# Performance work log

Hardware: AMD Instinct MI355X
Metric: run time of the kernel (lower is better)

Reference implementation:

```python
import jax, jax.numpy as jnp
import numpy as np
from jax import lax


def setup_inputs() -> dict:
    key = jax.random.key(0)
    kx, kw = jax.random.split(key)
    x = jax.random.normal(kx, (32, 3, 8192), dtype=jnp.float32)
    weight = jax.random.normal(kw, (128, 3, 64), dtype=jnp.float32)
    return {"x": x, "weight": weight}


def reference(x, weight):
    # x: [B, C, L], weight: [O, C, K]
    K = weight.shape[2]
    # Cross-correlation (conv1d, no bias, valid padding): [B, O, L-K+1]
    conv_out = lax.conv_general_dilated(
        x, weight, window_strides=(1,), padding='VALID',
        dimension_numbers=('NCH', 'OIH', 'NCH'))
    # Half squared norm of each shapelet: [O]
    w_norm = jnp.sum(weight ** 2, axis=(1, 2)) / 2
    # Half squared norm of each length-K window, via cumulative sums
    # (avoids materializing the [B, C, W, K] unfold tensor)
    sq = jnp.sum(x ** 2, axis=1)               # [B, L]
    c = jnp.pad(jnp.cumsum(sq, axis=1), ((0, 0), (1, 0)))  # [B, L+1]
    win_norm = (c[:, K:] - c[:, :-K]) / 2      # [B, L-K+1]
    # features = conv_out - (||w||^2/2 + ||window||^2/2)
    features = conv_out - w_norm[None, :, None] - win_norm[:, None, :]
    # global max-pool over time, then *(-2) -> min squared distance
    return -2.0 * jnp.max(features, axis=-1)   # [B, O]
```

## Files before the change

### kernel.cpp

```cpp
#include <hip/hip_runtime.h>
#include <hip/hip_bf16.h>
#include <float.h>

#define BB 32
#define LL 8192
#define OO 128
#define KK 64
#define WW (LL - KK + 1)
#define TCX 16

typedef __attribute__((ext_vector_type(8))) short short8;
typedef __attribute__((ext_vector_type(4))) float f32x4;

union AB { int4 i4; int i[4]; short8 v; };

static __device__ __forceinline__ unsigned int pkbf(float a, float b) {
    union { __hip_bfloat162 h; unsigned int u; } cv;
    cv.h = __float22bfloat162_rn(make_float2(a, b));
    return cv.u;
}

__global__ __launch_bounds__(256) void prep_kernel(const float* __restrict__ w,
                                                   unsigned short* __restrict__ wswz,
                                                   float* __restrict__ wn,
                                                   float* __restrict__ out) {
    int g = blockIdx.x * 256 + threadIdx.x;
    if (g < 3072) {
        int ob = g / 768;
        int rem = g - ob * 768;
        int rr = rem >> 5, o2 = rem & 31;
        int ks = rr >> 2, qp = rr & 3;
        int c = ks >> 1, h = ks & 1;
        const float* p = w + (size_t)(ob * 32 + o2) * 192 + c * 64 + h * 32 + qp * 8;
        float4 v0 = *(const float4*)p, v1 = *(const float4*)(p + 4);
        int4 pk;
        pk.x = (int)pkbf(v0.x, v0.y);
        pk.y = (int)pkbf(v0.z, v0.w);
        pk.z = (int)pkbf(v1.x, v1.y);
        pk.w = (int)pkbf(v1.z, v1.w);
        ((int4*)wswz)[g] = pk;
    }
    int oo = g - 3072;
    if (oo >= 0 && oo < OO) {
        const float* p = w + oo * 192;
        float s = 0.f;
        for (int i = 0; i < 192; ++i) { float v = p[i]; s = fmaf(v, v, s); }
        wn[oo] = 0.5f * s;
    }
    int oi = g - 3200;
    if (oi >= 0 && oi < BB * OO) out[oi] = 3.389e38f;
}

__global__ __launch_bounds__(256, 4) void shapeconv_main(const float* __restrict__ x,
                                                         const unsigned short* __restrict__ wswz,
                                                         const float* __restrict__ wn,
                                                         float* __restrict__ out) {
    __shared__ __align__(16) unsigned short w_lds[6144];
    __shared__ __align__(16) unsigned short xw_lds[4][576];
    __shared__ __align__(16) float sq_lds[4][192];
    __shared__ __align__(16) float P_lds[4][24];

    const int tcx = blockIdx.x;
    const int ob = blockIdx.y;
    const int b  = blockIdx.z;
    const int tid = threadIdx.x;
    const int wv = tid >> 6;
    const int lane = tid & 63;
    const int n  = lane & 15;
    const int qp = lane >> 4;
    const int T0w = (tcx * 4 + wv) * 128;

    float2 va[3], vb[3];
    const float* xb = x + (size_t)b * 3 * LL;
    {
        int e0 = T0w + 2 * lane;
        #pragma unroll
        for (int c = 0; c < 3; ++c) va[c] = *(const float2*)(xb + c * LL + e0);
        #pragma unroll
        for (int c = 0; c < 3; ++c) vb[c] = make_float2(0.f, 0.f);
        int e1 = T0w + 128 + 2 * lane;
        if (lane < 32 && e1 < LL) {
            #pragma unroll
            for (int c = 0; c < 3; ++c) vb[c] = *(const float2*)(xb + c * LL + e1);
        }
    }

    {
        const char* src = (const char*)wswz + (size_t)ob * 12288 + tid * 16;
        #pragma unroll
        for (int i = 0; i < 3; ++i) {
            __builtin_amdgcn_global_load_lds(
                (const __attribute__((address_space(1))) unsigned int*)(src + i * 4096),
                (__attribute__((address_space(3))) unsigned int*)((char*)w_lds + tid * 16 + i * 4096),
                16, 0, 0);
        }
    }

    float nw[2][4];
    #pragma unroll
    for (int ot = 0; ot < 2; ++ot)
        #pragma unroll
        for (int rg = 0; rg < 4; ++rg)
            nw[ot][rg] = wn[ob * 32 + 16 * ot + 4 * qp + rg];

    unsigned short* xw = xw_lds[wv];
    float* sqw = sq_lds[wv];
    float* Pw  = P_lds[wv];
    {
        float sx = 0.f, sy = 0.f;
        #pragma unroll
        for (int c = 0; c < 3; ++c) {
            *(unsigned int*)(xw + c * 192 + 2 * lane) = pkbf(va[c].x, va[c].y);
            sx = fmaf(va[c].x, va[c].x, sx);
            sy = fmaf(va[c].y, va[c].y, sy);
        }
        *(float2*)(sqw + 2 * lane) = make_float2(sx, sy);
        float p2 = sx + sy;
        p2 += __shfl_xor(p2, 1, 64);
        p2 += __shfl_xor(p2, 2, 64);
        if ((lane & 3) == 0) Pw[lane >> 2] = p2;
        float tx = 0.f, ty = 0.f;
        unsigned int pk[3];
        #pragma unroll
        for (int c = 0; c < 3; ++c) {
            tx = fmaf(vb[c].x, vb[c].x, tx);
            ty = fmaf(vb[c].y, vb[c].y, ty);
            pk[c] = pkbf(vb[c].x, vb[c].y);
        }
        if (lane < 32) {
            #pragma unroll
            for (int c = 0; c < 3; ++c) *(unsigned int*)(xw + c * 192 + 128 + 2 * lane) = pk[c];
            *(float2*)(sqw + 128 + 2 * lane) = make_float2(tx, ty);
        }
        float q2 = tx + ty;
        q2 += __shfl_xor(q2, 1, 64);
        q2 += __shfl_xor(q2, 2, 64);
        if (lane < 32 && (lane & 3) == 0) Pw[16 + (lane >> 2)] = q2;
    }

    __syncthreads();

    float wl[8];
    {
        float S = 0.f;
        #pragma unroll
        for (int i = 0; i < 8; ++i) S += Pw[n + i];
        #pragma unroll
        for (int r = 0; r < 8; ++r) {
            wl[r] = (T0w + 8 * n + r < WW) ? 0.5f * S : 1e30f;
            if (r < 7) S += sqw[8 * n + 64 + r] - sqw[8 * n + r];
        }
    }

    f32x4 acc[2][8];
    #pragma unroll
    for (int ot = 0; ot < 2; ++ot)
        #pragma unroll
        for (int rg = 0; rg < 4; ++rg)
            #pragma unroll
            for (int r = 0; r < 8; ++r)
                acc[ot][r][rg] = -nw[ot][rg] - wl[r];

    __builtin_amdgcn_s_setprio(1);
    #pragma unroll
    for (int ks = 0; ks < 6; ++ks) {
        int c = ks >> 1, h = ks & 1;
        int e0b = c * 384 + 64 * h + 16 * (n + qp);
        int4 Ea = *(const int4*)((const char*)xw + e0b);
        int4 Eb = *(const int4*)((const char*)xw + e0b + 16);
        int D[8] = {Ea.x, Ea.y, Ea.z, Ea.w, Eb.x, Eb.y, Eb.z, Eb.w};
        AB a0, a1;
        const int4* wq = (const int4*)w_lds + (ks * 4 + qp) * 32;
        a0.i4 = wq[n];
        a1.i4 = wq[16 + n];
        #pragma unroll
        for (int r = 0; r < 8; ++r) {
            AB bf;
            int s = r >> 1;
            if ((r & 1) == 0) {
                bf.i[0] = D[s]; bf.i[1] = D[s + 1]; bf.i[2] = D[s + 2]; bf.i[3] = D[s + 3];
            } else {
                #pragma unroll
                for (int d = 0; d < 4; ++d)
                    bf.i[d] = (int)__builtin_amdgcn_alignbit((unsigned)D[s + d + 1],
                                                             (unsigned)D[s + d], 16);
            }
            acc[0][r] = __builtin_amdgcn_mfma_f32_16x16x32_bf16(a0.v, bf.v, acc[0][r], 0, 0, 0);
            acc[1][r] = __builtin_amdgcn_mfma_f32_16x16x32_bf16(a1.v, bf.v, acc[1][r], 0, 0, 0);
        }
    }
    __builtin_amdgcn_s_setprio(0);

    #pragma unroll
    for (int ot = 0; ot < 2; ++ot)
        #pragma unroll
        for (int rg = 0; rg < 4; ++rg) {
            float mm = acc[ot][rg & 3][rg];
            mm = -FLT_MAX;
            #pragma unroll
            for (int r = 0; r < 8; ++r) mm = fmaxf(mm, acc[ot][r][rg]);
            #pragma unroll
            for (int s = 1; s <= 8; s <<= 1)
                mm = fmaxf(mm, __shfl_xor(mm, s, 64));
            if (n == 0) {
                atomicMin((int*)(out + (size_t)b * OO + ob * 32 + 16 * ot + 4 * qp + rg),
                          __float_as_int(-2.0f * mm));
            }
        }
}

extern "C" void kernel_launch(void* const* d_in, const int* in_sizes, int n_in,
                              void* d_out, int out_size, void* d_ws, size_t ws_size,
                              hipStream_t stream) {
    const float* x = (const float*)d_in[0];
    const float* w = (const float*)d_in[1];
    float* out = (float*)d_out;

    unsigned short* wswz = (unsigned short*)d_ws;
    float* wn = (float*)((char*)d_ws + 49152);

    prep_kernel<<<29, 256, 0, stream>>>(w, wswz, wn, out);
    dim3 grid(TCX, 4, BB);
    shapeconv_main<<<grid, 256, 0, stream>>>(x, wswz, wn, out);
}
```

Measured before the change: 81.01 us.

## Loop each wave over four time chunks with double-buffered x staging

Each wave now walks four consecutive 128-step time chunks and prefetches the next chunk's x into registers while the MFMAs for the current chunk run. Staging goes to double-buffered LDS and the running max is kept in registers, so atomics happen once per wave instead of once per chunk. Output channels per block drop from 32 to 16 (grid 4x8x32) to cut accumulator registers. The changes aim to amortize x loading, atomics and launch overhead, but each weight tile is now reused across fewer outputs per x load, and the chunk loop is serialized within a wave.

```diff
diff --git a/kernel.cpp b/kernel.cpp
--- a/kernel.cpp
+++ b/kernel.cpp
@@ -7,7 +7,7 @@
 #define OO 128
 #define KK 64
 #define WW (LL - KK + 1)
-#define TCX 16
+#define NCH 4
 
 typedef __attribute__((ext_vector_type(8))) short short8;
 typedef __attribute__((ext_vector_type(4))) float f32x4;
@@ -26,12 +26,12 @@
                                                    float* __restrict__ out) {
     int g = blockIdx.x * 256 + threadIdx.x;
     if (g < 3072) {
-        int ob = g / 768;
-        int rem = g - ob * 768;
-        int rr = rem >> 5, o2 = rem & 31;
+        int ob = g / 384;
+        int rem = g - ob * 384;
+        int rr = rem >> 4, o2 = rem & 15;
         int ks = rr >> 2, qp = rr & 3;
         int c = ks >> 1, h = ks & 1;
-        const float* p = w + (size_t)(ob * 32 + o2) * 192 + c * 64 + h * 32 + qp * 8;
+        const float* p = w + (size_t)(ob * 16 + o2) * 192 + c * 64 + h * 32 + qp * 8;
         float4 v0 = *(const float4*)p, v1 = *(const float4*)(p + 4);
         int4 pk;
         pk.x = (int)pkbf(v0.x, v0.y);
@@ -51,16 +51,63 @@
     if (oi >= 0 && oi < BB * OO) out[oi] = 3.389e38f;
 }
 
+static __device__ __forceinline__ void stage_load(const float* __restrict__ xb, int T0,
+                                                  int lane, float2* va, float2* vb) {
+    int e0 = T0 + 2 * lane;
+    #pragma unroll
+    for (int c = 0; c < 3; ++c) va[c] = *(const float2*)(xb + c * LL + e0);
+    #pragma unroll
+    for (int c = 0; c < 3; ++c) vb[c] = make_float2(0.f, 0.f);
+    int e1 = T0 + 128 + 2 * lane;
+    if (lane < 32 && e1 < LL) {
+        #pragma unroll
+        for (int c = 0; c < 3; ++c) vb[c] = *(const float2*)(xb + c * LL + e1);
+    }
+}
+
+static __device__ __forceinline__ void stage_store(int lane, const float2* va, const float2* vb,
+                                                   unsigned short* xw, float* sqw, float* Pw) {
+    float sx = 0.f, sy = 0.f;
+    #pragma unroll
+    for (int c = 0; c < 3; ++c) {
+        *(unsigned int*)(xw + c * 192 + 2 * lane) = pkbf(va[c].x, va[c].y);
+        sx = fmaf(va[c].x, va[c].x, sx);
+        sy = fmaf(va[c].y, va[c].y, sy);
+    }
+    *(float2*)(sqw + 2 * lane) = make_float2(sx, sy);
+    float p2 = sx + sy;
+    p2 += __shfl_xor(p2, 1, 64);
+    p2 += __shfl_xor(p2, 2, 64);
+    if ((lane & 3) == 0) Pw[lane >> 2] = p2;
+    float tx = 0.f, ty = 0.f;
+    unsigned int pk[3];
+    #pragma unroll
+    for (int c = 0; c < 3; ++c) {
+        tx = fmaf(vb[c].x, vb[c].x, tx);
+        ty = fmaf(vb[c].y, vb[c].y, ty);
+        pk[c] = pkbf(vb[c].x, vb[c].y);
+    }
+    if (lane < 32) {
+        #pragma unroll
+        for (int c = 0; c < 3; ++c) *(unsigned int*)(xw + c * 192 + 128 + 2 * lane) = pk[c];
+        *(float2*)(sqw + 128 + 2 * lane) = make_float2(tx, ty);
+    }
+    float q2 = tx + ty;
+    q2 += __shfl_xor(q2, 1, 64);
+    q2 += __shfl_xor(q2, 2, 64);
+    if (lane < 32 && (lane & 3) == 0) Pw[16 + (lane >> 2)] = q2;
+}
+
 __global__ __launch_bounds__(256, 4) void shapeconv_main(const float* __restrict__ x,
                                                          const unsigned short* __restrict__ wswz,
                                                          const float* __restrict__ wn,
                                                          float* __restrict__ out) {
-    __shared__ __align__(16) unsigned short w_lds[6144];
-    __shared__ __align__(16) unsigned short xw_lds[4][576];
-    __shared__ __align__(16) float sq_lds[4][192];
-    __shared__ __align__(16) float P_lds[4][24];
-
-    const int tcx = blockIdx.x;
+    __shared__ __align__(16) unsigned short w_lds[3072];
+    __shared__ __align__(16) unsigned short xw_lds[4][2][576];
+    __shared__ __align__(16) float sq_lds[4][2][192];
+    __shared__ __align__(16) float P_lds[4][2][24];
+
+    const int tg = blockIdx.x;
     const int ob = blockIdx.y;
     const int b  = blockIdx.z;
     const int tid = threadIdx.x;
@@ -68,145 +115,119 @@
     const int lane = tid & 63;
     const int n  = lane & 15;
     const int qp = lane >> 4;
-    const int T0w = (tcx * 4 + wv) * 128;
+    const int Tw = tg * 2048 + wv * 512;
+    const float* xb = x + (size_t)b * 3 * LL;
 
     float2 va[3], vb[3];
-    const float* xb = x + (size_t)b * 3 * LL;
+    stage_load(xb, Tw, lane, va, vb);
+
     {
-        int e0 = T0w + 2 * lane;
-        #pragma unroll
-        for (int c = 0; c < 3; ++c) va[c] = *(const float2*)(xb + c * LL + e0);
-        #pragma unroll
-        for (int c = 0; c < 3; ++c) vb[c] = make_float2(0.f, 0.f);
-        int e1 = T0w + 128 + 2 * lane;
-        if (lane < 32 && e1 < LL) {
-            #pragma unroll
-            for (int c = 0; c < 3; ++c) vb[c] = *(const float2*)(xb + c * LL + e1);
-        }
-    }
-
-    {
-        const char* src = (const char*)wswz + (size_t)ob * 12288 + tid * 16;
-        #pragma unroll
-        for (int i = 0; i < 3; ++i) {
+        const char* src = (const char*)wswz + (size_t)ob * 6144;
+        __builtin_amdgcn_global_load_lds(
+            (const __attribute__((address_space(1))) unsigned int*)(src + tid * 16),
+            (__attribute__((address_space(3))) unsigned int*)((char*)w_lds + tid * 16),
+            16, 0, 0);
+        if (tid < 128)
             __builtin_amdgcn_global_load_lds(
-                (const __attribute__((address_space(1))) unsigned int*)(src + i * 4096),
-                (__attribute__((address_space(3))) unsigned int*)((char*)w_lds + tid * 16 + i * 4096),
+                (const __attribute__((address_space(1))) unsigned int*)(src + 4096 + tid * 16),
+                (__attribute__((address_space(3))) unsigned int*)((char*)w_lds + 4096 + tid * 16),
                 16, 0, 0);
-        }
-    }
-
-    float nw[2][4];
-    #pragma unroll
-    for (int ot = 0; ot < 2; ++ot)
-        #pragma unroll
-        for (int rg = 0; rg < 4; ++rg)
-            nw[ot][rg] = wn[ob * 32 + 16 * ot + 4 * qp + rg];
-
-    unsigned short* xw = xw_lds[wv];
-    float* sqw = sq_lds[wv];
-    float* Pw  = P_lds[wv];
-    {
-        float sx = 0.f, sy = 0.f;
-        #pragma unroll
-        for (int c = 0; c < 3; ++c) {
-            *(unsigned int*)(xw + c * 192 + 2 * lane) = pkbf(va[c].x, va[c].y);
-            sx = fmaf(va[c].x, va[c].x, sx);
-            sy = fmaf(va[c].y, va[c].y, sy);
-        }
-        *(float2*)(sqw + 2 * lane) = make_float2(sx, sy);
-        float p2 = sx + sy;
-        p2 += __shfl_xor(p2, 1, 64);
-        p2 += __shfl_xor(p2, 2, 64);
-        if ((lane & 3) == 0) Pw[lane >> 2] = p2;
-        float tx = 0.f, ty = 0.f;
-        unsigned int pk[3];
-        #pragma unroll
-        for (int c = 0; c < 3; ++c) {
-            tx = fmaf(vb[c].x, vb[c].x, tx);
-            ty = fmaf(vb[c].y, vb[c].y, ty);
-            pk[c] = pkbf(vb[c].x, vb[c].y);
-        }
-        if (lane < 32) {
-            #pragma unroll
-            for (int c = 0; c < 3; ++c) *(unsigned int*)(xw + c * 192 + 128 + 2 * lane) = pk[c];
-            *(float2*)(sqw + 128 + 2 * lane) = make_float2(tx, ty);
-        }
-        float q2 = tx + ty;
-        q2 += __shfl_xor(q2, 1, 64);
-        q2 += __shfl_xor(q2, 2, 64);
-        if (lane < 32 && (lane & 3) == 0) Pw[16 + (lane >> 2)] = q2;
-    }
+    }
+
+    float nw4[4];
+    #pragma unroll
+    for (int rg = 0; rg < 4; ++rg) nw4[rg] = wn[ob * 16 + 4 * qp + rg];
+
+    unsigned short* xw0 = xw_lds[wv][0];
+    float* sq0 = sq_lds[wv][0];
+    float* Pw0 = P_lds[wv][0];
+    stage_store(lane, va, vb, xw0, sq0, Pw0);
 
     __syncthreads();
 
-    float wl[8];
-    {
-        float S = 0.f;
-        #pragma unroll
-        for (int i = 0; i < 8; ++i) S += Pw[n + i];
-        #pragma unroll
-        for (int r = 0; r < 8; ++r) {
-            wl[r] = (T0w + 8 * n + r < WW) ? 0.5f * S : 1e30f;
-            if (r < 7) S += sqw[8 * n + 64 + r] - sqw[8 * n + r];
-        }
-    }
-
-    f32x4 acc[2][8];
-    #pragma unroll
-    for (int ot = 0; ot < 2; ++ot)
-        #pragma unroll
-        for (int rg = 0; rg < 4; ++rg)
-            #pragma unroll
-            for (int r = 0; r < 8; ++r)
-                acc[ot][r][rg] = -nw[ot][rg] - wl[r];
-
-    __builtin_amdgcn_s_setprio(1);
-    #pragma unroll
-    for (int ks = 0; ks < 6; ++ks) {
-        int c = ks >> 1, h = ks & 1;
-        int e0b = c * 384 + 64 * h + 16 * (n + qp);
-        int4 Ea = *(const int4*)((const char*)xw + e0b);
-        int4 Eb = *(const int4*)((const char*)xw + e0b + 16);
-        int D[8] = {Ea.x, Ea.y, Ea.z, Ea.w, Eb.x, Eb.y, Eb.z, Eb.w};
-        AB a0, a1;
-        const int4* wq = (const int4*)w_lds + (ks * 4 + qp) * 32;
-        a0.i4 = wq[n];
-        a1.i4 = wq[16 + n];
-        #pragma unroll
-        for (int r = 0; r < 8; ++r) {
-            AB bf;
-            int s = r >> 1;
-            if ((r & 1) == 0) {
-                bf.i[0] = D[s]; bf.i[1] = D[s + 1]; bf.i[2] = D[s + 2]; bf.i[3] = D[s + 3];
-            } else {
-                #pragma unroll
-                for (int d = 0; d < 4; ++d)
-                    bf.i[d] = (int)__builtin_amdgcn_alignbit((unsigned)D[s + d + 1],
-                                                             (unsigned)D[s + d], 16);
+    float m2[4];
+    #pragma unroll
+    for (int rg = 0; rg < 4; ++rg) m2[rg] = -FLT_MAX;
+
+    for (int ci = 0; ci < NCH; ++ci) {
+        const int bs = ci & 1;
+        const int T0 = Tw + ci * 128;
+        const bool more = (ci + 1 < NCH);
+        if (more) stage_load(xb, T0 + 128, lane, va, vb);
+
+        unsigned short* xw = xw_lds[wv][bs];
+        float* sqw = sq_lds[wv][bs];
+        float* Pw  = P_lds[wv][bs];
+
+        float wl[8];
+        {
+            float S = 0.f;
+            #pragma unroll
+            for (int i = 0; i < 8; ++i) S += Pw[n + i];
+            #pragma unroll
+            for (int r = 0; r < 8; ++r) {
+                wl[r] = (T0 + 8 * n + r < WW) ? 0.5f * S : 1e30f;
+                if (r < 7) S += sqw[8 * n + 64 + r] - sqw[8 * n + r];
             }
-            acc[0][r] = __builtin_amdgcn_mfma_f32_16x16x32_bf16(a0.v, bf.v, acc[0][r], 0, 0, 0);
-            acc[1][r] = __builtin_amdgcn_mfma_f32_16x16x32_bf16(a1.v, bf.v, acc[1][r], 0, 0, 0);
-        }
-    }
-    __builtin_amdgcn_s_setprio(0);
-
-    #pragma unroll
-    for (int ot = 0; ot < 2; ++ot)
+        }
+
+        f32x4 acc[8];
+        #pragma unroll
+        for (int r = 0; r < 8; ++r)
+            #pragma unroll
+            for (int rg = 0; rg < 4; ++rg)
+                acc[r][rg] = -nw4[rg] - wl[r];
+
+        __builtin_amdgcn_s_setprio(1);
+        #pragma unroll
+        for (int ks = 0; ks < 6; ++ks) {
+            int c = ks >> 1, h = ks & 1;
+            int e0b = c * 384 + 64 * h + 16 * (n + qp);
+            int4 Ea = *(const int4*)((const char*)xw + e0b);
+            int4 Eb = *(const int4*)((const char*)xw + e0b + 16);
+            int D[8] = {Ea.x, Ea.y, Ea.z, Ea.w, Eb.x, Eb.y, Eb.z, Eb.w};
+            AB a0;
+            a0.i4 = ((const int4*)w_lds)[(ks * 4 + qp) * 16 + n];
+            #pragma unroll
+            for (int r = 0; r < 8; ++r) {
+                AB bf;
+                int s = r >> 1;
+                if ((r & 1) == 0) {
+                    bf.i[0] = D[s]; bf.i[1] = D[s + 1]; bf.i[2] = D[s + 2]; bf.i[3] = D[s + 3];
+                } else {
+                    #pragma unroll
+                    for (int d = 0; d < 4; ++d)
+                        bf.i[d] = (int)__builtin_amdgcn_alignbit((unsigned)D[s + d + 1],
+                                                                 (unsigned)D[s + d], 16);
+                }
+                acc[r] = __builtin_amdgcn_mfma_f32_16x16x32_bf16(a0.v, bf.v, acc[r], 0, 0, 0);
+            }
+        }
+        __builtin_amdgcn_s_setprio(0);
+
         #pragma unroll
         for (int rg = 0; rg < 4; ++rg) {
-            float mm = acc[ot][rg & 3][rg];
-            mm = -FLT_MAX;
-            #pragma unroll
-            for (int r = 0; r < 8; ++r) mm = fmaxf(mm, acc[ot][r][rg]);
-            #pragma unroll
-            for (int s = 1; s <= 8; s <<= 1)
-                mm = fmaxf(mm, __shfl_xor(mm, s, 64));
-            if (n == 0) {
-                atomicMin((int*)(out + (size_t)b * OO + ob * 32 + 16 * ot + 4 * qp + rg),
-                          __float_as_int(-2.0f * mm));
-            }
-        }
+            float mm = m2[rg];
+            #pragma unroll
+            for (int r = 0; r < 8; ++r) mm = fmaxf(mm, acc[r][rg]);
+            m2[rg] = mm;
+        }
+
+        if (more)
+            stage_store(lane, va, vb, xw_lds[wv][1 - bs], sq_lds[wv][1 - bs], P_lds[wv][1 - bs]);
+    }
+
+    #pragma unroll
+    for (int rg = 0; rg < 4; ++rg) {
+        float mm = m2[rg];
+        #pragma unroll
+        for (int s = 1; s <= 8; s <<= 1)
+            mm = fmaxf(mm, __shfl_xor(mm, s, 64));
+        if (n == 0) {
+            atomicMin((int*)(out + (size_t)b * OO + ob * 16 + 4 * qp + rg),
+                      __float_as_int(-2.0f * mm));
+        }
+    }
 }
 
 extern "C" void kernel_launch(void* const* d_in, const int* in_sizes, int n_in,
@@ -220,6 +241,6 @@
     float* wn = (float*)((char*)d_ws + 49152);
 
     prep_kernel<<<29, 256, 0, stream>>>(w, wswz, wn, out);
-    dim3 grid(TCX, 4, BB);
+    dim3 grid(4, 8, BB);
     shapeconv_main<<<grid, 256, 0, stream>>>(x, wswz, wn, out);
 }
```

New measurement: 73.81 us. 8.9% less time.
